# Kernel tuning notes

Hardware: AMD Instinct MI355X
Metric: run time of the kernel (lower is better)

The kernel has to match this reference:

```python
import jax, jax.numpy as jnp
import numpy as np

P = 113          # vocab (modulus)
D = 128          # residual_dim
H = 4            # n_heads (hardcoded in Model)
DH = D // H      # head_dim = 32
HID = 4 * D      # mlp hidden = 512
BATCH = 131072
RATE = 0.5       # attention_rate


def setup_inputs() -> dict:
    key = jax.random.key(0)
    ks = jax.random.split(key, 12)
    std = 1.0 / D ** 0.5
    x = jax.random.randint(ks[0], (BATCH, 2), 0, P)
    tok_emb = jax.random.normal(ks[1], (P, D), jnp.float32) / D ** 0.5
    pos_emb = jax.random.normal(ks[2], (2, D), jnp.float32) / D ** 0.5
    W_Q = jax.random.normal(ks[3], (H, D, DH), jnp.float32) * std
    W_K = jax.random.normal(ks[4], (H, D, DH), jnp.float32) * std
    W_V = jax.random.normal(ks[5], (H, D, DH), jnp.float32) * std
    W_O = jax.random.normal(ks[6], (H, DH, D), jnp.float32) * std
    # nn.Linear default init: U(-1/sqrt(fan_in), 1/sqrt(fan_in))
    b1_bound = 1.0 / D ** 0.5
    W1 = jax.random.uniform(ks[7], (D, HID), jnp.float32, -b1_bound, b1_bound)
    b1 = jax.random.uniform(ks[8], (HID,), jnp.float32, -b1_bound, b1_bound)
    b2_bound = 1.0 / HID ** 0.5
    W2 = jax.random.uniform(ks[9], (HID, D), jnp.float32, -b2_bound, b2_bound)
    b2 = jax.random.uniform(ks[10], (D,), jnp.float32, -b2_bound, b2_bound)
    W_U = jax.random.normal(ks[11], (P, D), jnp.float32) / P ** 0.5
    return dict(x=x, tok_emb=tok_emb, pos_emb=pos_emb, W_Q=W_Q, W_K=W_K,
                W_V=W_V, W_O=W_O, W1=W1, b1=b1, W2=W2, b2=b2, W_U=W_U)


def reference(x, tok_emb, pos_emb, W_Q, W_K, W_V, W_O, W1, b1, W2, b2, W_U):
    # embed: [B,2,D]
    resid = tok_emb[x] + pos_emb[None, :, :]
    # attention
    q = jnp.einsum('bpd,hdk->bphk', resid, W_Q)
    k = jnp.einsum('bpd,hdk->bphk', resid, W_K)
    v = jnp.einsum('bpd,hdk->bphk', resid, W_V)
    scores = jnp.einsum('bqhk,bshk->bhqs', q, k) / DH ** 0.5  # [B,H,2,2]
    pattern = jax.nn.softmax(scores, axis=-1)
    pattern = (1.0 - RATE) + RATE * pattern  # uniform blend, no causal mask
    z = jnp.einsum('bshk,bhqs->bqhk', v, pattern)
    attn_out = jnp.einsum('bqhk,hkd->bqd', z, W_O)
    resid = resid + attn_out
    # mlp
    h = jax.nn.relu(resid @ W1 + b1)
    resid = resid + (h @ W2 + b2)
    # unembed: [B,2,P]
    logits = jnp.einsum('vd,bpd->bpv', W_U, resid)
    return logits
```

## Files before the change

kernel.cpp:

```cpp
#include <hip/hip_runtime.h>
#include <hip/hip_bf16.h>
#include <stdint.h>

typedef __hip_bfloat16 bf16;
typedef __attribute__((ext_vector_type(8))) short short8;
typedef __attribute__((ext_vector_type(4))) float float4v;
typedef __attribute__((ext_vector_type(2))) float f2v;

#define NVOCAB 113
#define NPAIR (113 * 113)
#define DDIM 128
#define HIDDIM 512
#define PAIRS_PB 16
#define ROWS_PB 32

#define OFF_B1  145792
#define OFF_B2  211840

#define BOFF_WOT 0
#define BOFF_W1T 16384
#define BOFF_W2T (16384 + 65536)
#define BOFF_WUP (16384 + 65536 + 65536)
#define BTOTAL   (16384 + 65536 + 65536 + 16384)

__device__ __forceinline__ uint16_t f2b(float f) {
  bf16 h = __float2bfloat16(f);
  return *(uint16_t*)&h;
}
__device__ __forceinline__ float b2f(uint16_t u) {
  return __uint_as_float(((uint32_t)u) << 16);
}
__device__ __forceinline__ float ldsrc(const void* p, int i, int isb) {
  return isb ? b2f(((const uint16_t*)p)[i]) : ((const float*)p)[i];
}

__device__ __forceinline__ int detect_isb(const uint32_t* __restrict__ tok_raw) {
  uint32_t u = tok_raw[threadIdx.x & 63];
  int e = (u >> 7) & 0xff;
  unsigned long long m = __ballot(e >= 100 && e <= 126);
  return __popcll(m) >= 48;
}

struct SrcPtrs { const void* p[11]; };

__global__ void __launch_bounds__(384) build_kernel(
    SrcPtrs sp, float* __restrict__ wf,
    float* __restrict__ resid_pre, float* __restrict__ qt,
    float* __restrict__ kt, float* __restrict__ vt,
    uint16_t* __restrict__ wb) {
  const int tid = threadIdx.x;
  const int blk = blockIdx.x;
  const int isb = detect_isb((const uint32_t*)sp.p[0]);

  if (blk < 226) {
    const int row = blk;
    const int t = row >> 1, p = row & 1;
    __shared__ float r[DDIM];
    if (tid < DDIM) {
      float rv = ldsrc(sp.p[0], t * DDIM + tid, isb) +
                 ldsrc(sp.p[1], p * DDIM + tid, isb);
      r[tid] = rv;
      resid_pre[row * DDIM + tid] = rv;
    }
    __syncthreads();
    const int which = tid >> 7, jj = tid & 127;
    const int h = jj >> 5, j = jj & 31;
    const void* wsrc = sp.p[2 + which];
    const int base = h * 4096 + j;
    float a = 0.f;
    if (isb) {
      const uint16_t* w16 = (const uint16_t*)wsrc;
      #pragma unroll 8
      for (int d = 0; d < 128; ++d)
        a += r[d] * b2f(w16[base + d * 32]);
    } else {
      const float* w32 = (const float*)wsrc;
      #pragma unroll 8
      for (int d = 0; d < 128; ++d)
        a += r[d] * w32[base + d * 32];
    }
    float* outp = (which == 0) ? qt : (which == 1) ? kt : vt;
    outp[row * DDIM + jj] = a;
  } else if (blk < 653) {
    const int idx = (blk - 226) * 384 + tid;
    if (idx < BTOTAL) {
      float v;
      if (idx < BOFF_W1T) {
        int l = idx, d = l >> 7, c = l & 127;
        v = ldsrc(sp.p[5], c * 128 + d, isb);
      } else if (idx < BOFF_W2T) {
        int l = idx - BOFF_W1T, n = l >> 7, d = l & 127;
        v = ldsrc(sp.p[6], d * 512 + n, isb);
      } else if (idx < BOFF_WUP) {
        int l = idx - BOFF_W2T, d = l >> 9, j = l & 511;
        v = ldsrc(sp.p[8], j * 128 + d, isb);
      } else {
        int l = idx - BOFF_WUP, vv = l >> 7, d = l & 127;
        v = (vv < NVOCAB) ? ldsrc(sp.p[10], vv * 128 + d, isb) : 0.f;
      }
      wb[idx] = f2b(v);
    }
  } else {
    const int i = (blk - 653) * 384 + tid;
    if (i < 512) wf[OFF_B1 + i] = ldsrc(sp.p[7], i, isb);
    else if (i < 640) wf[OFF_B2 + (i - 512)] = ldsrc(sp.p[9], i - 512, isb);
  }
}

__global__ void __launch_bounds__(512, 3) pair_mfma_kernel(
    const float* __restrict__ resid_pre, const float* __restrict__ qt,
    const float* __restrict__ kt, const float* __restrict__ vt,
    const float* __restrict__ wf, const uint16_t* __restrict__ wb,
    float* __restrict__ table) {
  __shared__ uint16_t bufH[ROWS_PB * 512];
  __shared__ uint16_t bufZ[ROWS_PB * 128];
  __shared__ uint16_t bufS[ROWS_PB * 128];
  __shared__ float    spat[PAIRS_PB * 16];

  const int tid = threadIdx.x;
  const int blk = blockIdx.x;
  const int lane = tid & 63;
  const int npar = tid >> 6;
  const int l15 = lane & 15, quad = lane >> 4;

  #define ROW_OF(row_) ({                                        \
    int pr_ = blk * PAIRS_PB + ((row_) >> 1);                    \
    if (pr_ >= NPAIR) pr_ = NPAIR - 1;                           \
    int t0_ = pr_ / NVOCAB, t1_ = pr_ - t0_ * NVOCAB;            \
    ((row_) & 1) ? t1_ * 2 + 1 : t0_ * 2; })

  const int nG = npar * 16 + l15;
  float rpre[2][4];
  #pragma unroll
  for (int mf = 0; mf < 2; ++mf)
    #pragma unroll
    for (int r = 0; r < 4; ++r)
      rpre[mf][r] = resid_pre[ROW_OF(mf * 16 + quad * 4 + r) * DDIM + nG];
  float bias1v[4];
  #pragma unroll
  for (int ni = 0; ni < 4; ++ni)
    bias1v[ni] = wf[OFF_B1 + (npar + ni * 8) * 16 + l15];
  const float bias2 = wf[OFF_B2 + nG];
  const int zm = tid >> 4, zc0 = (tid & 15) * 8;
  float4 zv0a, zv0b, zv1a, zv1b;
  {
    const int zr0 = ROW_OF((zm >> 1) * 2);
    const int zr1 = ROW_OF((zm >> 1) * 2 + 1);
    const float4* p0 = (const float4*)(vt + zr0 * DDIM + zc0);
    const float4* p1 = (const float4*)(vt + zr1 * DDIM + zc0);
    zv0a = p0[0]; zv0b = p0[1]; zv1a = p1[0]; zv1b = p1[1];
  }

  if (tid < 256) {
    const int pl = tid >> 4, s = tid & 15;
    const int pair = blk * PAIRS_PB + pl;
    if (pair < NPAIR) {
      const int t0 = pair / NVOCAB, t1 = pair - t0 * NVOCAB;
      const int row0 = t0 * 2, row1 = t1 * 2 + 1;
      const int h = s >> 2, qp = (s >> 1) & 1, spp = s & 1;
      const float4* qrow = (const float4*)(qt + (qp ? row1 : row0) * DDIM + h * 32);
      const float4* krow = (const float4*)(kt + (spp ? row1 : row0) * DDIM + h * 32);
      float acc = 0.f;
      #pragma unroll
      for (int j = 0; j < 8; ++j) {
        float4 qv = qrow[j], kv = krow[j];
        acc += qv.x * kv.x + qv.y * kv.y + qv.z * kv.z + qv.w * kv.w;
      }
      spat[pl * 16 + s] = acc * 0.17677669529663687f;
    } else {
      spat[pl * 16 + s] = 0.f;
    }
  }
  __syncthreads();

  if (tid < 128) {
    const int pl = tid >> 3, s = tid & 7;
    const int base = pl * 16 + s * 2;
    float s0 = spat[base], s1 = spat[base + 1];
    float m = fmaxf(s0, s1);
    float e0 = __expf(s0 - m), e1 = __expf(s1 - m);
    float inv = 1.f / (e0 + e1);
    spat[base]     = 0.5f + 0.5f * e0 * inv;
    spat[base + 1] = 0.5f + 0.5f * e1 * inv;
  }
  __syncthreads();

  {
    const int pl = zm >> 1, qp = zm & 1;
    const int h = zc0 >> 5;
    const float p0 = spat[pl * 16 + h * 4 + qp * 2];
    const float p1 = spat[pl * 16 + h * 4 + qp * 2 + 1];
    float v0[8] = {zv0a.x, zv0a.y, zv0a.z, zv0a.w, zv0b.x, zv0b.y, zv0b.z, zv0b.w};
    float v1[8] = {zv1a.x, zv1a.y, zv1a.z, zv1a.w, zv1b.x, zv1b.y, zv1b.z, zv1b.w};
    short8 pk;
    #pragma unroll
    for (int e = 0; e < 8; ++e)
      pk[e] = (short)f2b(p0 * v0[e] + p1 * v1[e]);
    *(short8*)&bufZ[(zm * 16 + ((zc0 >> 3) ^ (zm & 15))) * 8] = pk;
  }
  __syncthreads();

  float smid[2][4];

  {
    short8 af[2][4];
    #pragma unroll
    for (int mf = 0; mf < 2; ++mf)
      #pragma unroll
      for (int ks = 0; ks < 4; ++ks)
        af[mf][ks] = *(const short8*)&bufZ[((mf * 16 + l15) * 16 +
                                           ((ks * 4 + quad) ^ l15)) * 8];
    short8 bW[4];
    {
      const uint16_t* bp = wb + BOFF_WOT + nG * 128 + quad * 8;
      #pragma unroll
      for (int ks = 0; ks < 4; ++ks)
        bW[ks] = *(const short8*)(bp + ks * 32);
    }
    float4v acc[2] = {{0.f, 0.f, 0.f, 0.f}, {0.f, 0.f, 0.f, 0.f}};
    #pragma unroll
    for (int mf = 0; mf < 2; ++mf)
      #pragma unroll
      for (int ks = 0; ks < 4; ++ks)
        acc[mf] = __builtin_amdgcn_mfma_f32_16x16x32_bf16(af[mf][ks], bW[ks],
                                                          acc[mf], 0, 0, 0);
    #pragma unroll
    for (int mf = 0; mf < 2; ++mf)
      #pragma unroll
      for (int r = 0; r < 4; ++r) {
        const int row = mf * 16 + quad * 4 + r;
        float v = acc[mf][r] + rpre[mf][r];
        smid[mf][r] = v;
        bufS[(row * 16 + ((nG >> 3) ^ (row & 15))) * 8 + (nG & 7)] = f2b(v);
      }
  }
  __syncthreads();

  {
    short8 af[2][4];
    #pragma unroll
    for (int mf = 0; mf < 2; ++mf)
      #pragma unroll
      for (int ks = 0; ks < 4; ++ks)
        af[mf][ks] = *(const short8*)&bufS[((mf * 16 + l15) * 16 +
                                           ((ks * 4 + quad) ^ l15)) * 8];
    #pragma unroll
    for (int half = 0; half < 2; ++half) {
      short8 bW[2][4];
      #pragma unroll
      for (int nj = 0; nj < 2; ++nj) {
        const int ni = half * 2 + nj;
        const int n = (npar + ni * 8) * 16 + l15;
        const uint16_t* bp = wb + BOFF_W1T + n * 128 + quad * 8;
        #pragma unroll
        for (int ks = 0; ks < 4; ++ks)
          bW[nj][ks] = *(const short8*)(bp + ks * 32);
      }
      #pragma unroll
      for (int nj = 0; nj < 2; ++nj) {
        const int ni = half * 2 + nj;
        const int n = (npar + ni * 8) * 16 + l15;
        float4v acc[2] = {{0.f, 0.f, 0.f, 0.f}, {0.f, 0.f, 0.f, 0.f}};
        #pragma unroll
        for (int mf = 0; mf < 2; ++mf)
          #pragma unroll
          for (int ks = 0; ks < 4; ++ks)
            acc[mf] = __builtin_amdgcn_mfma_f32_16x16x32_bf16(
                af[mf][ks], bW[nj][ks], acc[mf], 0, 0, 0);
        const float bias = bias1v[ni];
        #pragma unroll
        for (int mf = 0; mf < 2; ++mf)
          #pragma unroll
          for (int r = 0; r < 4; ++r) {
            const int row = mf * 16 + quad * 4 + r;
            bufH[(row * 64 + ((n >> 3) ^ (row & 15))) * 8 + (n & 7)] =
                f2b(fmaxf(acc[mf][r] + bias, 0.f));
          }
      }
    }
  }
  __syncthreads();

  {
    const uint16_t* bp = wb + BOFF_W2T + nG * 512 + quad * 8;
    float4v acc0 = {0.f, 0.f, 0.f, 0.f};
    float4v acc1 = {0.f, 0.f, 0.f, 0.f};
    #pragma unroll
    for (int half = 0; half < 2; ++half) {
      short8 bB[8];
      #pragma unroll
      for (int k8 = 0; k8 < 8; ++k8)
        bB[k8] = *(const short8*)(bp + (half * 8 + k8) * 32);
      #pragma unroll
      for (int qtr = 0; qtr < 2; ++qtr) {
        short8 a0[4], a1[4];
        #pragma unroll
        for (int k4 = 0; k4 < 4; ++k4) {
          const int ks = half * 8 + qtr * 4 + k4;
          a0[k4] = *(const short8*)&bufH[(l15 * 64 +
                                         ((ks * 4 + quad) ^ l15)) * 8];
          a1[k4] = *(const short8*)&bufH[((16 + l15) * 64 +
                                         ((ks * 4 + quad) ^ l15)) * 8];
        }
        #pragma unroll
        for (int k4 = 0; k4 < 4; ++k4) {
          acc0 = __builtin_amdgcn_mfma_f32_16x16x32_bf16(
              a0[k4], bB[qtr * 4 + k4], acc0, 0, 0, 0);
          acc1 = __builtin_amdgcn_mfma_f32_16x16x32_bf16(
              a1[k4], bB[qtr * 4 + k4], acc1, 0, 0, 0);
        }
      }
    }
    #pragma unroll
    for (int r = 0; r < 4; ++r) {
      const int row0 = quad * 4 + r;
      const int row1 = 16 + quad * 4 + r;
      bufZ[(row0 * 16 + ((nG >> 3) ^ (row0 & 15))) * 8 + (nG & 7)] =
          f2b(acc0[r] + bias2 + smid[0][r]);
      bufZ[(row1 * 16 + ((nG >> 3) ^ (row1 & 15))) * 8 + (nG & 7)] =
          f2b(acc1[r] + bias2 + smid[1][r]);
    }
  }
  __syncthreads();

  {
    short8 ar[2][4];
    #pragma unroll
    for (int mf = 0; mf < 2; ++mf)
      #pragma unroll
      for (int ks = 0; ks < 4; ++ks)
        ar[mf][ks] = *(const short8*)&bufZ[((mf * 16 + l15) * 16 +
                                           ((ks * 4 + quad) ^ l15)) * 8];
    short8 bW[4];
    {
      const uint16_t* bp = wb + BOFF_WUP + nG * 128 + quad * 8;
      #pragma unroll
      for (int ks = 0; ks < 4; ++ks)
        bW[ks] = *(const short8*)(bp + ks * 32);
    }
    float4v acc[2] = {{0.f, 0.f, 0.f, 0.f}, {0.f, 0.f, 0.f, 0.f}};
    #pragma unroll
    for (int mf = 0; mf < 2; ++mf)
      #pragma unroll
      for (int ks = 0; ks < 4; ++ks)
        acc[mf] = __builtin_amdgcn_mfma_f32_16x16x32_bf16(ar[mf][ks], bW[ks],
                                                          acc[mf], 0, 0, 0);
    if (nG < NVOCAB) {
      #pragma unroll
      for (int mf = 0; mf < 2; ++mf)
        #pragma unroll
        for (int r = 0; r < 4; ++r) {
          const int row = mf * 16 + quad * 4 + r;
          const int pair = blk * PAIRS_PB + (row >> 1);
          if (pair < NPAIR)
            table[pair * 226 + (row & 1) * 113 + nG] = acc[mf][r];
        }
    }
  }
  #undef ROW_OF
}

__global__ void gather_kernel(const uint32_t* __restrict__ x_raw,
                              const f2v* __restrict__ table2,
                              f2v* __restrict__ out2, int total) {
  uint32_t xs = x_raw[2 * (threadIdx.x & 63) + 1];
  unsigned long long nz = __ballot(xs != 0u);
  const int is64 = (nz == 0ull);

  const int i = blockIdx.x * 256 + threadIdx.x;
  if (i >= total) return;
  const int b = i / NVOCAB;
  const int j = i - b * NVOCAB;
  int t0, t1;
  if (is64) {
    t0 = (int)x_raw[4 * b];
    t1 = (int)x_raw[4 * b + 2];
  } else {
    t0 = (int)x_raw[2 * b];
    t1 = (int)x_raw[2 * b + 1];
  }
  t0 = min(max(t0, 0), NVOCAB - 1);
  t1 = min(max(t1, 0), NVOCAB - 1);
  const int pair = t0 * NVOCAB + t1;
  f2v v = table2[(size_t)pair * NVOCAB + j];
  __builtin_nontemporal_store(v, &out2[i]);
}

extern "C" void kernel_launch(void* const* d_in, const int* in_sizes, int n_in,
                              void* d_out, int out_size, void* d_ws, size_t ws_size,
                              hipStream_t stream) {
  float*    wf        = (float*)((char*)d_ws + 256);
  float*    resid_pre = (float*)((char*)d_ws + 905984);
  float*    qt        = (float*)((char*)d_ws + 1021696);
  float*    kt        = (float*)((char*)d_ws + 1137408);
  float*    vt        = (float*)((char*)d_ws + 1253120);
  float*    table     = (float*)((char*)d_ws + 1368832);
  uint16_t* wb        = (uint16_t*)((char*)d_ws + 12912016);

  const int B = in_sizes[0] / 2;

  SrcPtrs sp;
  for (int i = 0; i < 11; ++i) sp.p[i] = d_in[i + 1];

  build_kernel<<<655, 384, 0, stream>>>(sp, wf, resid_pre, qt, kt, vt, wb);

  const int nblk = (NPAIR + PAIRS_PB - 1) / PAIRS_PB;
  pair_mfma_kernel<<<nblk, 512, 0, stream>>>(resid_pre, qt, kt, vt, wf, wb,
                                             table);

  const int total = B * NVOCAB;
  gather_kernel<<<(total + 255) / 256, 256, 0, stream>>>(
      (const uint32_t*)d_in[0], (const f2v*)table, (f2v*)d_out, total);
}
```

Before: 245.7 us.

## Prefetch next-stage weight fragments across barriers and relax launch bounds

```diff
diff --git a/kernel.cpp b/kernel.cpp
--- a/kernel.cpp
+++ b/kernel.cpp
@@ -107,7 +107,7 @@
   }
 }
 
-__global__ void __launch_bounds__(512, 3) pair_mfma_kernel(
+__global__ void __launch_bounds__(512, 2) pair_mfma_kernel(
     const float* __restrict__ resid_pre, const float* __restrict__ qt,
     const float* __restrict__ kt, const float* __restrict__ vt,
     const float* __restrict__ wf, const uint16_t* __restrict__ wb,
@@ -130,6 +130,14 @@
     ((row_) & 1) ? t1_ * 2 + 1 : t0_ * 2; })
 
   const int nG = npar * 16 + l15;
+
+  short8 bW0[4];
+  {
+    const uint16_t* bp = wb + BOFF_WOT + nG * 128 + quad * 8;
+    #pragma unroll
+    for (int ks = 0; ks < 4; ++ks) bW0[ks] = *(const short8*)(bp + ks * 32);
+  }
+
   float rpre[2][4];
   #pragma unroll
   for (int mf = 0; mf < 2; ++mf)
@@ -201,6 +209,7 @@
   __syncthreads();
 
   float smid[2][4];
+  short8 bW1a[2][4];
 
   {
     short8 af[2][4];
@@ -210,20 +219,21 @@
       for (int ks = 0; ks < 4; ++ks)
         af[mf][ks] = *(const short8*)&bufZ[((mf * 16 + l15) * 16 +
                                            ((ks * 4 + quad) ^ l15)) * 8];
-    short8 bW[4];
-    {
-      const uint16_t* bp = wb + BOFF_WOT + nG * 128 + quad * 8;
-      #pragma unroll
-      for (int ks = 0; ks < 4; ++ks)
-        bW[ks] = *(const short8*)(bp + ks * 32);
-    }
     float4v acc[2] = {{0.f, 0.f, 0.f, 0.f}, {0.f, 0.f, 0.f, 0.f}};
     #pragma unroll
     for (int mf = 0; mf < 2; ++mf)
       #pragma unroll
       for (int ks = 0; ks < 4; ++ks)
-        acc[mf] = __builtin_amdgcn_mfma_f32_16x16x32_bf16(af[mf][ks], bW[ks],
+        acc[mf] = __builtin_amdgcn_mfma_f32_16x16x32_bf16(af[mf][ks], bW0[ks],
                                                           acc[mf], 0, 0, 0);
+    #pragma unroll
+    for (int nj = 0; nj < 2; ++nj) {
+      const int n = (npar + nj * 8) * 16 + l15;
+      const uint16_t* bp = wb + BOFF_W1T + n * 128 + quad * 8;
+      #pragma unroll
+      for (int ks = 0; ks < 4; ++ks)
+        bW1a[nj][ks] = *(const short8*)(bp + ks * 32);
+    }
     #pragma unroll
     for (int mf = 0; mf < 2; ++mf)
       #pragma unroll
@@ -236,6 +246,8 @@
   }
   __syncthreads();
 
+  short8 bB2a[8];
+
   {
     short8 af[2][4];
     #pragma unroll
@@ -245,71 +257,116 @@
         af[mf][ks] = *(const short8*)&bufS[((mf * 16 + l15) * 16 +
                                            ((ks * 4 + quad) ^ l15)) * 8];
     #pragma unroll
-    for (int half = 0; half < 2; ++half) {
-      short8 bW[2][4];
-      #pragma unroll
-      for (int nj = 0; nj < 2; ++nj) {
-        const int ni = half * 2 + nj;
-        const int n = (npar + ni * 8) * 16 + l15;
-        const uint16_t* bp = wb + BOFF_W1T + n * 128 + quad * 8;
+    for (int nj = 0; nj < 2; ++nj) {
+      const int ni = nj;
+      const int n = (npar + ni * 8) * 16 + l15;
+      float4v acc[2] = {{0.f, 0.f, 0.f, 0.f}, {0.f, 0.f, 0.f, 0.f}};
+      #pragma unroll
+      for (int mf = 0; mf < 2; ++mf)
         #pragma unroll
         for (int ks = 0; ks < 4; ++ks)
-          bW[nj][ks] = *(const short8*)(bp + ks * 32);
-      }
-      #pragma unroll
-      for (int nj = 0; nj < 2; ++nj) {
-        const int ni = half * 2 + nj;
-        const int n = (npar + ni * 8) * 16 + l15;
-        float4v acc[2] = {{0.f, 0.f, 0.f, 0.f}, {0.f, 0.f, 0.f, 0.f}};
+          acc[mf] = __builtin_amdgcn_mfma_f32_16x16x32_bf16(
+              af[mf][ks], bW1a[nj][ks], acc[mf], 0, 0, 0);
+      const float bias = bias1v[ni];
+      #pragma unroll
+      for (int mf = 0; mf < 2; ++mf)
         #pragma unroll
-        for (int mf = 0; mf < 2; ++mf)
-          #pragma unroll
-          for (int ks = 0; ks < 4; ++ks)
-            acc[mf] = __builtin_amdgcn_mfma_f32_16x16x32_bf16(
-                af[mf][ks], bW[nj][ks], acc[mf], 0, 0, 0);
-        const float bias = bias1v[ni];
+        for (int r = 0; r < 4; ++r) {
+          const int row = mf * 16 + quad * 4 + r;
+          bufH[(row * 64 + ((n >> 3) ^ (row & 15))) * 8 + (n & 7)] =
+              f2b(fmaxf(acc[mf][r] + bias, 0.f));
+        }
+    }
+    short8 bW1b[2][4];
+    #pragma unroll
+    for (int nj = 0; nj < 2; ++nj) {
+      const int n = (npar + (2 + nj) * 8) * 16 + l15;
+      const uint16_t* bp = wb + BOFF_W1T + n * 128 + quad * 8;
+      #pragma unroll
+      for (int ks = 0; ks < 4; ++ks)
+        bW1b[nj][ks] = *(const short8*)(bp + ks * 32);
+    }
+    #pragma unroll
+    for (int nj = 0; nj < 2; ++nj) {
+      const int ni = 2 + nj;
+      const int n = (npar + ni * 8) * 16 + l15;
+      float4v acc[2] = {{0.f, 0.f, 0.f, 0.f}, {0.f, 0.f, 0.f, 0.f}};
+      #pragma unroll
+      for (int mf = 0; mf < 2; ++mf)
         #pragma unroll
-        for (int mf = 0; mf < 2; ++mf)
-          #pragma unroll
-          for (int r = 0; r < 4; ++r) {
-            const int row = mf * 16 + quad * 4 + r;
-            bufH[(row * 64 + ((n >> 3) ^ (row & 15))) * 8 + (n & 7)] =
-                f2b(fmaxf(acc[mf][r] + bias, 0.f));
-          }
-      }
-    }
-  }
-  __syncthreads();
+        for (int ks = 0; ks < 4; ++ks)
+          acc[mf] = __builtin_amdgcn_mfma_f32_16x16x32_bf16(
+              af[mf][ks], bW1b[nj][ks], acc[mf], 0, 0, 0);
+      const float bias = bias1v[ni];
+      #pragma unroll
+      for (int mf = 0; mf < 2; ++mf)
+        #pragma unroll
+        for (int r = 0; r < 4; ++r) {
+          const int row = mf * 16 + quad * 4 + r;
+          bufH[(row * 64 + ((n >> 3) ^ (row & 15))) * 8 + (n & 7)] =
+              f2b(fmaxf(acc[mf][r] + bias, 0.f));
+        }
+    }
+    {
+      const uint16_t* bp = wb + BOFF_W2T + nG * 512 + quad * 8;
+      #pragma unroll
+      for (int k8 = 0; k8 < 8; ++k8)
+        bB2a[k8] = *(const short8*)(bp + k8 * 32);
+    }
+  }
+  __syncthreads();
+
+  short8 bW3[4];
 
   {
     const uint16_t* bp = wb + BOFF_W2T + nG * 512 + quad * 8;
     float4v acc0 = {0.f, 0.f, 0.f, 0.f};
     float4v acc1 = {0.f, 0.f, 0.f, 0.f};
     #pragma unroll
-    for (int half = 0; half < 2; ++half) {
-      short8 bB[8];
-      #pragma unroll
-      for (int k8 = 0; k8 < 8; ++k8)
-        bB[k8] = *(const short8*)(bp + (half * 8 + k8) * 32);
-      #pragma unroll
-      for (int qtr = 0; qtr < 2; ++qtr) {
-        short8 a0[4], a1[4];
-        #pragma unroll
-        for (int k4 = 0; k4 < 4; ++k4) {
-          const int ks = half * 8 + qtr * 4 + k4;
-          a0[k4] = *(const short8*)&bufH[(l15 * 64 +
-                                         ((ks * 4 + quad) ^ l15)) * 8];
-          a1[k4] = *(const short8*)&bufH[((16 + l15) * 64 +
-                                         ((ks * 4 + quad) ^ l15)) * 8];
-        }
-        #pragma unroll
-        for (int k4 = 0; k4 < 4; ++k4) {
-          acc0 = __builtin_amdgcn_mfma_f32_16x16x32_bf16(
-              a0[k4], bB[qtr * 4 + k4], acc0, 0, 0, 0);
-          acc1 = __builtin_amdgcn_mfma_f32_16x16x32_bf16(
-              a1[k4], bB[qtr * 4 + k4], acc1, 0, 0, 0);
-        }
-      }
+    for (int qtr = 0; qtr < 2; ++qtr) {
+      short8 a0[4], a1[4];
+      #pragma unroll
+      for (int k4 = 0; k4 < 4; ++k4) {
+        const int ks = qtr * 4 + k4;
+        a0[k4] = *(const short8*)&bufH[(l15 * 64 + ((ks * 4 + quad) ^ l15)) * 8];
+        a1[k4] = *(const short8*)&bufH[((16 + l15) * 64 +
+                                       ((ks * 4 + quad) ^ l15)) * 8];
+      }
+      #pragma unroll
+      for (int k4 = 0; k4 < 4; ++k4) {
+        acc0 = __builtin_amdgcn_mfma_f32_16x16x32_bf16(
+            a0[k4], bB2a[qtr * 4 + k4], acc0, 0, 0, 0);
+        acc1 = __builtin_amdgcn_mfma_f32_16x16x32_bf16(
+            a1[k4], bB2a[qtr * 4 + k4], acc1, 0, 0, 0);
+      }
+    }
+    short8 bB2b[8];
+    #pragma unroll
+    for (int k8 = 0; k8 < 8; ++k8)
+      bB2b[k8] = *(const short8*)(bp + (8 + k8) * 32);
+    #pragma unroll
+    for (int qtr = 0; qtr < 2; ++qtr) {
+      short8 a0[4], a1[4];
+      #pragma unroll
+      for (int k4 = 0; k4 < 4; ++k4) {
+        const int ks = 8 + qtr * 4 + k4;
+        a0[k4] = *(const short8*)&bufH[(l15 * 64 + ((ks * 4 + quad) ^ l15)) * 8];
+        a1[k4] = *(const short8*)&bufH[((16 + l15) * 64 +
+                                       ((ks * 4 + quad) ^ l15)) * 8];
+      }
+      #pragma unroll
+      for (int k4 = 0; k4 < 4; ++k4) {
+        acc0 = __builtin_amdgcn_mfma_f32_16x16x32_bf16(
+            a0[k4], bB2b[qtr * 4 + k4], acc0, 0, 0, 0);
+        acc1 = __builtin_amdgcn_mfma_f32_16x16x32_bf16(
+            a1[k4], bB2b[qtr * 4 + k4], acc1, 0, 0, 0);
+      }
+    }
+    {
+      const uint16_t* bp3 = wb + BOFF_WUP + nG * 128 + quad * 8;
+      #pragma unroll
+      for (int ks = 0; ks < 4; ++ks)
+        bW3[ks] = *(const short8*)(bp3 + ks * 32);
     }
     #pragma unroll
     for (int r = 0; r < 4; ++r) {
@@ -331,19 +388,12 @@
       for (int ks = 0; ks < 4; ++ks)
         ar[mf][ks] = *(const short8*)&bufZ[((mf * 16 + l15) * 16 +
                                            ((ks * 4 + quad) ^ l15)) * 8];
-    short8 bW[4];
-    {
-      const uint16_t* bp = wb + BOFF_WUP + nG * 128 + quad * 8;
-      #pragma unroll
-      for (int ks = 0; ks < 4; ++ks)
-        bW[ks] = *(const short8*)(bp + ks * 32);
-    }
     float4v acc[2] = {{0.f, 0.f, 0.f, 0.f}, {0.f, 0.f, 0.f, 0.f}};
     #pragma unroll
     for (int mf = 0; mf < 2; ++mf)
       #pragma unroll
       for (int ks = 0; ks < 4; ++ks)
-        acc[mf] = __builtin_amdgcn_mfma_f32_16x16x32_bf16(ar[mf][ks], bW[ks],
+        acc[mf] = __builtin_amdgcn_mfma_f32_16x16x32_bf16(ar[mf][ks], bW3[ks],
                                                           acc[mf], 0, 0, 0);
     if (nG < NVOCAB) {
       #pragma unroll
```

Measured after the change: 242.7 us. Within noise of the previous version (-1.2%).
